# Optimization experiments

Hardware: AMD Instinct MI355X
Metric: run time of the kernel (lower is better)

The kernel has to match this reference:

```python
import jax, jax.numpy as jnp
import numpy as np

HEADS = 8
DIM_HEAD = 32
DIM = 256
HIDDEN = HEADS * DIM_HEAD  # 256


def setup_inputs() -> dict:
    key = jax.random.key(0)
    ks = jax.random.split(key, 6)
    B, T, C, H, W = 4, 16, DIM, 32, 32
    x = jax.random.normal(ks[0], (B, T, C, H, W), dtype=jnp.float32)
    rel_pos = jax.random.normal(ks[1], (HEADS, T, T), dtype=jnp.float32)
    # 1x1 conv weights == channel-mixing matrices
    w_qkv = jax.random.normal(ks[2], (3 * HIDDEN, C), dtype=jnp.float32) * (C ** -0.5)
    b_qkv = jnp.zeros((3 * HIDDEN,), dtype=jnp.float32)
    w_out = jax.random.normal(ks[3], (C, HIDDEN), dtype=jnp.float32) * (HIDDEN ** -0.5)
    b_out = jnp.zeros((C,), dtype=jnp.float32)
    return {"x": x, "rel_pos": rel_pos, "w_qkv": w_qkv, "b_qkv": b_qkv,
            "w_out": w_out, "b_out": b_out}


def reference(x, rel_pos, w_qkv, b_qkv, w_out, b_out):
    B, T, C, H, W = x.shape
    scale = DIM_HEAD ** -0.5
    # 1x1 conv QKV projection: (B,T,C,H,W) x (3*hidden, C) -> (B,T,H,W,3*hidden)
    qkv = jnp.einsum('btchw,oc->bthwo', x, w_qkv) + b_qkv
    q, k, v = jnp.split(qkv, 3, axis=-1)
    # split heads: (B,T,H,W,heads,dim_head); attention over T per (b,h,w,head)
    q = q.reshape(B, T, H, W, HEADS, DIM_HEAD) * scale
    k = k.reshape(B, T, H, W, HEADS, DIM_HEAD)
    v = v.reshape(B, T, H, W, HEADS, DIM_HEAD)
    # sim: (B,H,W,heads,T,T)
    sim = jnp.einsum('bihwnd,bjhwnd->bhwnij', q, k)
    sim = sim + rel_pos  # (heads,T,T) broadcasts over (B,H,W)
    attn = jax.nn.softmax(sim, axis=-1)
    out = jnp.einsum('bhwnij,bjhwnd->bihwnd', attn, v)  # (B,T,H,W,heads,dh)
    out = out.reshape(B, T, H, W, HIDDEN)
    # 1x1 conv output projection back to C channels
    y = jnp.einsum('bthwe,ce->bthwc', out, w_out) + b_out
    return jnp.transpose(y, (0, 1, 4, 2, 3))  # (B,T,C,H,W)
```

## Files before the change

### kernel.cpp

```cpp
#include <hip/hip_runtime.h>
#include <hip/hip_bf16.h>

typedef __attribute__((ext_vector_type(8))) short bf16x8;
typedef __attribute__((ext_vector_type(4))) float f32x4;
typedef __attribute__((ext_vector_type(16))) float f32x16;

namespace {

__device__ __forceinline__ unsigned short f2bf(float f) {
  unsigned int x;
  __builtin_memcpy(&x, &f, 4);
  x += 0x7fff + ((x >> 16) & 1);
  return (unsigned short)(x >> 16);
}
__device__ __forceinline__ unsigned int pack2(float a, float b) {
  return (unsigned int)f2bf(a) | ((unsigned int)f2bf(b) << 16);
}

constexpr int kWBStride = 264;
constexpr int kWBTile = 32 * kWBStride;
constexpr int kWB = 2 * kWBTile;
constexpr int kSite = 1824;
constexpr int kSmem = kWB + 8 * kSite;
constexpr int kPanelStride = 72;
static_assert(kSmem * 2 <= 65536, "LDS budget");
static_assert(16 * 16 * kPanelStride <= kSmem, "x panel fits");
static_assert(512 * 17 * 4 <= kSmem * 2, "fbuf fits");

__global__ __launch_bounds__(512, 2) void attn_fused(
    const float* __restrict__ x,
    const float* __restrict__ rel,
    const float* __restrict__ wqkv,
    const float* __restrict__ bqkv,
    const float* __restrict__ wout,
    const float* __restrict__ bout,
    float* __restrict__ out) {
  __shared__ __align__(16) unsigned short smem[kSmem];
  const int tid = threadIdx.x;
  const int lane = tid & 63;
  const int wave = tid >> 6;
  const int quad = lane >> 4;
  const int lrow = lane & 15;
  const int half = lane >> 5;
  const int n32 = lane & 31;
  const int b = blockIdx.x >> 6;
  const int hw0 = (blockIdx.x & 63) * 16;

  const int wrow = tid >> 4;
  const int wcol = (tid & 15) * 16;
  float4 pw[4];
  {
    const float* sp = wqkv + (size_t)wrow * 256 + wcol;
#pragma unroll
    for (int u = 0; u < 4; ++u) pw[u] = *(const float4*)(sp + u * 4);
  }

  bf16x8 ax[16];
  {
    unsigned short* panel = smem;
    const int sloc = wave * 2 + (n32 >> 4);
#pragma unroll
    for (int cc4 = 0; cc4 < 4; ++cc4) {
      const int c0 = cc4 * 64;
      __syncthreads();
#pragma unroll
      for (int u = 0; u < 8; ++u) {
        const int idx = u * 512 + tid;
        const int row = idx >> 2;
        const int q = idx & 3;
        const int t = row >> 6;
        const int cl = row & 63;
        const float4 v = *(const float4*)(
            x + (((size_t)(b * 16 + t) * 256 + c0 + cl) << 10) + hw0 + q * 4);
        unsigned short* pr = panel + (t * 16 + q * 4) * kPanelStride + cl;
        pr[0] = f2bf(v.x);
        pr[kPanelStride] = f2bf(v.y);
        pr[2 * kPanelStride] = f2bf(v.z);
        pr[3 * kPanelStride] = f2bf(v.w);
      }
      __syncthreads();
#pragma unroll
      for (int kk = 0; kk < 4; ++kk)
        ax[cc4 * 4 + kk] = *(const bf16x8*)(
            panel + (lrow * 16 + sloc) * kPanelStride + kk * 16 + half * 8);
    }
  }

  unsigned short* qb = smem + kWB + wave * kSite;
  unsigned short* kb = qb + 640;
  unsigned short* vt = qb + 1280;

  const f32x4 zero4 = {0.f, 0.f, 0.f, 0.f};
  const float scale = 0.17677669529663687f;
  bf16x8 ao[2][8];

  auto qkv_tile = [&](int g, float bias) -> f32x16 {
    __syncthreads();
    unsigned short* WBc = smem + (g & 1) * kWBTile;
    {
      unsigned short* dst = WBc + wrow * kWBStride + wcol;
      uint4 a, bq;
      a.x = pack2(pw[0].x, pw[0].y);
      a.y = pack2(pw[0].z, pw[0].w);
      a.z = pack2(pw[1].x, pw[1].y);
      a.w = pack2(pw[1].z, pw[1].w);
      bq.x = pack2(pw[2].x, pw[2].y);
      bq.y = pack2(pw[2].z, pw[2].w);
      bq.z = pack2(pw[3].x, pw[3].y);
      bq.w = pack2(pw[3].z, pw[3].w);
      *(uint4*)dst = a;
      *(uint4*)(dst + 8) = bq;
    }
    {
      const int gn = g + 1;
      const int rowbase = (gn % 3) * 256 + (gn / 3) * 32;
      const float* sp = wqkv + (size_t)(rowbase + wrow) * 256 + wcol;
#pragma unroll
      for (int u = 0; u < 4; ++u) pw[u] = *(const float4*)(sp + u * 4);
    }
    __syncthreads();
    f32x16 acc;
#pragma unroll
    for (int i = 0; i < 16; ++i) acc[i] = bias;
    const unsigned short* br = WBc + n32 * kWBStride + half * 8;
#pragma unroll
    for (int ks = 0; ks < 16; ++ks) {
      const bf16x8 bf = *(const bf16x8*)(br + ks * 16);
      acc = __builtin_amdgcn_mfma_f32_32x32x16_bf16(ax[ks], bf, acc, 0, 0, 0);
    }
    return acc;
  };

  auto head_body = [&](int h) {
    const f32x16 qacc = qkv_tile(h * 3 + 0, bqkv[h * 32 + n32]);
    const f32x16 kacc = qkv_tile(h * 3 + 1, bqkv[256 + h * 32 + n32]);
    const f32x16 vacc = qkv_tile(h * 3 + 2, bqkv[512 + h * 32 + n32]);
    float rl[4];
#pragma unroll
    for (int r = 0; r < 4; ++r) rl[r] = rel[h * 256 + (quad * 4 + r) * 16 + lrow];

#pragma unroll
    for (int s = 0; s < 2; ++s) {
#pragma unroll
      for (int rr = 0; rr < 8; ++rr) {
        const int t = (rr & 3) + 8 * (rr >> 2) + 4 * half;
        qb[t * 40 + n32] = f2bf(qacc[8 * s + rr]);
        kb[t * 40 + n32] = f2bf(kacc[8 * s + rr]);
      }
#pragma unroll
      for (int rp = 0; rp < 4; ++rp) {
        const int rr = rp * 2;
        const int t = (rr & 3) + 8 * (rr >> 2) + 4 * half;
        *(unsigned int*)&vt[n32 * 16 + t] =
            pack2(vacc[8 * s + rr], vacc[8 * s + rr + 1]);
      }
      const bf16x8 qf = *(const bf16x8*)(qb + lrow * 40 + quad * 8);
      const bf16x8 kf = *(const bf16x8*)(kb + lrow * 40 + quad * 8);
      const f32x4 sim = __builtin_amdgcn_mfma_f32_16x16x32_bf16(qf, kf, zero4, 0, 0, 0);
      float p[4], inv[4];
#pragma unroll
      for (int r = 0; r < 4; ++r) {
        const float v = sim[r] * scale + rl[r];
        float m = v;
        for (int off = 8; off; off >>= 1) m = fmaxf(m, __shfl_xor(m, off));
        const float e = __expf(v - m);
        float sum = e;
        for (int off = 8; off; off >>= 1) sum += __shfl_xor(sum, off);
        p[r] = e;
        inv[r] = 1.0f / sum;
      }
      unsigned short* pb = kb;
#pragma unroll
      for (int r = 0; r < 4; ++r) pb[(quad * 4 + r) * 24 + lrow] = f2bf(p[r]);
      bf16x8 pf, vf0, vf1;
      if (quad < 2) {
        pf = *(const bf16x8*)(pb + lrow * 24 + quad * 8);
        vf0 = *(const bf16x8*)(vt + lrow * 16 + quad * 8);
        vf1 = *(const bf16x8*)(vt + (16 + lrow) * 16 + quad * 8);
      } else {
#pragma unroll
        for (int j = 0; j < 8; ++j) { pf[j] = 0; vf0[j] = 0; vf1[j] = 0; }
      }
      const f32x4 o0 = __builtin_amdgcn_mfma_f32_16x16x32_bf16(pf, vf0, zero4, 0, 0, 0);
      const f32x4 o1 = __builtin_amdgcn_mfma_f32_16x16x32_bf16(pf, vf1, zero4, 0, 0, 0);
#pragma unroll
      for (int r = 0; r < 4; ++r) {
        const int t = quad * 4 + r;
        qb[t * 40 + lrow] = f2bf(o0[r] * inv[r]);
        qb[t * 40 + 16 + lrow] = f2bf(o1[r] * inv[r]);
      }
      ao[s][h] = *(const bf16x8*)(qb + lrow * 40 + quad * 8);
    }
  };

  head_body(0);
  head_body(1);
  head_body(2);
  head_body(3);
  head_body(4);
  head_body(5);
  head_body(6);
  head_body(7);

  __syncthreads();
  float* fbuf = (float*)smem;
  float* ob = out + ((size_t)b << 22);
#pragma unroll 1
  for (int cc = 0; cc < 8; ++cc) {
#pragma unroll
    for (int sub = 0; sub < 2; ++sub) {
      const int c = cc * 32 + sub * 16 + lrow;
      const float bias = bout[c];
      f32x4 y0 = {bias, bias, bias, bias};
      f32x4 y1 = {bias, bias, bias, bias};
#pragma unroll
      for (int ks = 0; ks < 8; ++ks) {
        const float4 w0 = *(const float4*)(wout + (size_t)c * 256 + ks * 32 + quad * 8);
        const float4 w1 = *(const float4*)(wout + (size_t)c * 256 + ks * 32 + quad * 8 + 4);
        bf16x8 wf;
        wf[0] = (short)f2bf(w0.x); wf[1] = (short)f2bf(w0.y);
        wf[2] = (short)f2bf(w0.z); wf[3] = (short)f2bf(w0.w);
        wf[4] = (short)f2bf(w1.x); wf[5] = (short)f2bf(w1.y);
        wf[6] = (short)f2bf(w1.z); wf[7] = (short)f2bf(w1.w);
        y0 = __builtin_amdgcn_mfma_f32_16x16x32_bf16(ao[0][ks], wf, y0, 0, 0, 0);
        y1 = __builtin_amdgcn_mfma_f32_16x16x32_bf16(ao[1][ks], wf, y1, 0, 0, 0);
      }
#pragma unroll
      for (int r = 0; r < 4; ++r) {
        const int t = quad * 4 + r;
        const int L = (t * 32 + sub * 16 + lrow) * 17 + wave * 2;
        fbuf[L] = y0[r];
        fbuf[L + 1] = y1[r];
      }
    }
    __syncthreads();
    {
      const int t = tid >> 5, cl = tid & 31;
      float v[16];
#pragma unroll
      for (int i = 0; i < 16; ++i) v[i] = fbuf[tid * 17 + i];
      float* dst = ob + ((size_t)(t * 256 + cc * 32 + cl)) * 1024 + hw0;
#pragma unroll
      for (int u = 0; u < 4; ++u) {
        float4 q;
        q.x = v[u * 4]; q.y = v[u * 4 + 1]; q.z = v[u * 4 + 2]; q.w = v[u * 4 + 3];
        *(float4*)(dst + u * 4) = q;
      }
    }
    __syncthreads();
  }
}

}

extern "C" void kernel_launch(void* const* d_in, const int* in_sizes, int n_in,
                              void* d_out, int out_size, void* d_ws, size_t ws_size,
                              hipStream_t stream) {
  const float* x = (const float*)d_in[0];
  const float* rel = (const float*)d_in[1];
  const float* wqkv = (const float*)d_in[2];
  const float* bqkv = (const float*)d_in[3];
  const float* wout = (const float*)d_in[4];
  const float* bout = (const float*)d_in[5];
  float* out = (float*)d_out;
  (void)in_sizes; (void)n_in; (void)out_size; (void)d_ws; (void)ws_size;

  attn_fused<<<256, 512, 0, stream>>>(x, rel, wqkv, bqkv, wout, bout, out);
}
```

Measured before the change: 245.5 us.

## Software-pipeline x loads, stage W_out in LDS, double-buffer output epilogue

Prefetches the next x channel chunk into registers while the current chunk is converted into the LDS panel. Hoists the qkv and output biases into registers. Replaces per-lane global reads and bf16 conversion of W_out with a cooperative, double-buffered LDS staging of W_out tiles. The output staging buffer is also double-buffered so the store of one channel block overlaps the MFMA work of the next, halving the barriers per block. LDS use grows past 64KiB and launch bounds drop to one block per CU, which reduces occupancy.

```diff
diff --git a/kernel.cpp b/kernel.cpp
--- a/kernel.cpp
+++ b/kernel.cpp
@@ -21,13 +21,17 @@
 constexpr int kWBTile = 32 * kWBStride;
 constexpr int kWB = 2 * kWBTile;
 constexpr int kSite = 1824;
-constexpr int kSmem = kWB + 8 * kSite;
+constexpr int kSmemMain = kWB + 8 * kSite;
 constexpr int kPanelStride = 72;
-static_assert(kSmem * 2 <= 65536, "LDS budget");
-static_assert(16 * 16 * kPanelStride <= kSmem, "x panel fits");
-static_assert(512 * 17 * 4 <= kSmem * 2, "fbuf fits");
-
-__global__ __launch_bounds__(512, 2) void attn_fused(
+constexpr int kFb1 = 17408;
+constexpr int kWt0 = 34816;
+constexpr int kWt1 = kWt0 + kWBTile;
+constexpr int kSmem = kWt1 + kWBTile;
+static_assert(kSmem * 2 <= 160 * 1024, "LDS within 160KiB/CU");
+static_assert(kSmemMain <= kSmem, "main region fits");
+static_assert(16 * 16 * kPanelStride <= kSmemMain, "x panel fits");
+
+__global__ __launch_bounds__(512, 1) void attn_fused(
     const float* __restrict__ x,
     const float* __restrict__ rel,
     const float* __restrict__ wqkv,
@@ -59,10 +63,9 @@
   {
     unsigned short* panel = smem;
     const int sloc = wave * 2 + (n32 >> 4);
-#pragma unroll
-    for (int cc4 = 0; cc4 < 4; ++cc4) {
+    float4 rx[8];
+    auto loadChunk = [&](int cc4) {
       const int c0 = cc4 * 64;
-      __syncthreads();
 #pragma unroll
       for (int u = 0; u < 8; ++u) {
         const int idx = u * 512 + tid;
@@ -70,20 +73,42 @@
         const int q = idx & 3;
         const int t = row >> 6;
         const int cl = row & 63;
-        const float4 v = *(const float4*)(
+        rx[u] = *(const float4*)(
             x + (((size_t)(b * 16 + t) * 256 + c0 + cl) << 10) + hw0 + q * 4);
+      }
+    };
+    loadChunk(0);
+#pragma unroll
+    for (int cc4 = 0; cc4 < 4; ++cc4) {
+      __syncthreads();
+#pragma unroll
+      for (int u = 0; u < 8; ++u) {
+        const int idx = u * 512 + tid;
+        const int row = idx >> 2;
+        const int q = idx & 3;
+        const int t = row >> 6;
+        const int cl = row & 63;
         unsigned short* pr = panel + (t * 16 + q * 4) * kPanelStride + cl;
-        pr[0] = f2bf(v.x);
-        pr[kPanelStride] = f2bf(v.y);
-        pr[2 * kPanelStride] = f2bf(v.z);
-        pr[3 * kPanelStride] = f2bf(v.w);
-      }
+        pr[0] = f2bf(rx[u].x);
+        pr[kPanelStride] = f2bf(rx[u].y);
+        pr[2 * kPanelStride] = f2bf(rx[u].z);
+        pr[3 * kPanelStride] = f2bf(rx[u].w);
+      }
+      if (cc4 < 3) loadChunk(cc4 + 1);
       __syncthreads();
 #pragma unroll
       for (int kk = 0; kk < 4; ++kk)
         ax[cc4 * 4 + kk] = *(const bf16x8*)(
             panel + (lrow * 16 + sloc) * kPanelStride + kk * 16 + half * 8);
     }
+  }
+
+  float bq0[8], bk0[8], bv0[8];
+#pragma unroll
+  for (int h = 0; h < 8; ++h) {
+    bq0[h] = bqkv[h * 32 + n32];
+    bk0[h] = bqkv[256 + h * 32 + n32];
+    bv0[h] = bqkv[512 + h * 32 + n32];
   }
 
   unsigned short* qb = smem + kWB + wave * kSite;
@@ -132,9 +157,9 @@
   };
 
   auto head_body = [&](int h) {
-    const f32x16 qacc = qkv_tile(h * 3 + 0, bqkv[h * 32 + n32]);
-    const f32x16 kacc = qkv_tile(h * 3 + 1, bqkv[256 + h * 32 + n32]);
-    const f32x16 vacc = qkv_tile(h * 3 + 2, bqkv[512 + h * 32 + n32]);
+    const f32x16 qacc = qkv_tile(h * 3 + 0, bq0[h]);
+    const f32x16 kacc = qkv_tile(h * 3 + 1, bk0[h]);
+    const f32x16 vacc = qkv_tile(h * 3 + 2, bv0[h]);
     float rl[4];
 #pragma unroll
     for (int r = 0; r < 4; ++r) rl[r] = rel[h * 256 + (quad * 4 + r) * 16 + lrow];
@@ -202,43 +227,78 @@
   head_body(6);
   head_body(7);
 
+  float* fb0 = (float*)smem;
+  float* fb1 = (float*)(smem + kFb1);
+  unsigned short* wt0 = smem + kWt0;
+  unsigned short* wt1 = smem + kWt1;
+
+  float4 pwe[4];
+  auto loadWout = [&](int cc) {
+    const float* sp = wout + (size_t)(cc * 32 + wrow) * 256 + wcol;
+#pragma unroll
+    for (int u = 0; u < 4; ++u) pwe[u] = *(const float4*)(sp + u * 4);
+  };
+  auto writeWt = [&](unsigned short* wt) {
+    uint4 a, bq;
+    a.x = pack2(pwe[0].x, pwe[0].y);
+    a.y = pack2(pwe[0].z, pwe[0].w);
+    a.z = pack2(pwe[1].x, pwe[1].y);
+    a.w = pack2(pwe[1].z, pwe[1].w);
+    bq.x = pack2(pwe[2].x, pwe[2].y);
+    bq.y = pack2(pwe[2].z, pwe[2].w);
+    bq.z = pack2(pwe[3].x, pwe[3].y);
+    bq.w = pack2(pwe[3].z, pwe[3].w);
+    unsigned short* d = wt + wrow * kWBStride + wcol;
+    *(uint4*)d = a;
+    *(uint4*)(d + 8) = bq;
+  };
+
+  float bo0[8], bo1[8];
+#pragma unroll
+  for (int cc = 0; cc < 8; ++cc) {
+    bo0[cc] = bout[cc * 32 + lrow];
+    bo1[cc] = bout[cc * 32 + 16 + lrow];
+  }
+
+  loadWout(0);
+  writeWt(wt0);
+  loadWout(1);
   __syncthreads();
-  float* fbuf = (float*)smem;
+
   float* ob = out + ((size_t)b << 22);
-#pragma unroll 1
-  for (int cc = 0; cc < 8; ++cc) {
-#pragma unroll
-    for (int sub = 0; sub < 2; ++sub) {
-      const int c = cc * 32 + sub * 16 + lrow;
-      const float bias = bout[c];
-      f32x4 y0 = {bias, bias, bias, bias};
-      f32x4 y1 = {bias, bias, bias, bias};
-#pragma unroll
-      for (int ks = 0; ks < 8; ++ks) {
-        const float4 w0 = *(const float4*)(wout + (size_t)c * 256 + ks * 32 + quad * 8);
-        const float4 w1 = *(const float4*)(wout + (size_t)c * 256 + ks * 32 + quad * 8 + 4);
-        bf16x8 wf;
-        wf[0] = (short)f2bf(w0.x); wf[1] = (short)f2bf(w0.y);
-        wf[2] = (short)f2bf(w0.z); wf[3] = (short)f2bf(w0.w);
-        wf[4] = (short)f2bf(w1.x); wf[5] = (short)f2bf(w1.y);
-        wf[6] = (short)f2bf(w1.z); wf[7] = (short)f2bf(w1.w);
-        y0 = __builtin_amdgcn_mfma_f32_16x16x32_bf16(ao[0][ks], wf, y0, 0, 0, 0);
-        y1 = __builtin_amdgcn_mfma_f32_16x16x32_bf16(ao[1][ks], wf, y1, 0, 0, 0);
-      }
-#pragma unroll
-      for (int r = 0; r < 4; ++r) {
-        const int t = quad * 4 + r;
-        const int L = (t * 32 + sub * 16 + lrow) * 17 + wave * 2;
-        fbuf[L] = y0[r];
-        fbuf[L + 1] = y1[r];
-      }
-    }
-    __syncthreads();
-    {
+  auto epi = [&](int i) {
+    if (i < 8) {
+      unsigned short* wt = (i & 1) ? wt1 : wt0;
+      float* fb = (i & 1) ? fb1 : fb0;
+#pragma unroll
+      for (int sub = 0; sub < 2; ++sub) {
+        const float bias = sub ? bo1[i] : bo0[i];
+        f32x4 y0 = {bias, bias, bias, bias};
+        f32x4 y1 = {bias, bias, bias, bias};
+        const unsigned short* wrp = wt + (sub * 16 + lrow) * kWBStride;
+#pragma unroll
+        for (int ks = 0; ks < 8; ++ks) {
+          const bf16x8 wf = *(const bf16x8*)(wrp + ks * 32 + quad * 8);
+          y0 = __builtin_amdgcn_mfma_f32_16x16x32_bf16(ao[0][ks], wf, y0, 0, 0, 0);
+          y1 = __builtin_amdgcn_mfma_f32_16x16x32_bf16(ao[1][ks], wf, y1, 0, 0, 0);
+        }
+#pragma unroll
+        for (int r = 0; r < 4; ++r) {
+          const int L = ((quad * 4 + r) * 32 + sub * 16 + lrow) * 17 + wave * 2;
+          fb[L] = y0[r];
+          fb[L + 1] = y1[r];
+        }
+      }
+      if (i < 7) writeWt((i & 1) ? wt0 : wt1);
+      if (i < 6) loadWout(i + 2);
+    }
+    if (i > 0) {
+      const int cc = i - 1;
+      float* fb = ((i - 1) & 1) ? fb1 : fb0;
       const int t = tid >> 5, cl = tid & 31;
       float v[16];
 #pragma unroll
-      for (int i = 0; i < 16; ++i) v[i] = fbuf[tid * 17 + i];
+      for (int u = 0; u < 16; ++u) v[u] = fb[tid * 17 + u];
       float* dst = ob + ((size_t)(t * 256 + cc * 32 + cl)) * 1024 + hw0;
 #pragma unroll
       for (int u = 0; u < 4; ++u) {
@@ -247,8 +307,9 @@
         *(float4*)(dst + u * 4) = q;
       }
     }
-    __syncthreads();
-  }
+    if (i < 8) __syncthreads();
+  };
+  epi(0); epi(1); epi(2); epi(3); epi(4); epi(5); epi(6); epi(7); epi(8);
 }
 
 }
```

New measurement: 223.4 us. 9.0% less time.
